# Performance work log

Hardware: AMD Instinct MI355X
Metric: run time of the kernel (lower is better)

## Reference

```python
import jax, jax.numpy as jnp
import numpy as np

B, M, NT, V, D, H, E, S = 4, 12, 12, 10000, 64, 3, 512, 32


def setup_inputs() -> dict:
    key = jax.random.key(0)
    ks = jax.random.split(key, 16)
    def rn(k, shape, scale=0.05):
        return jax.random.normal(k, shape, dtype=jnp.float32) * scale
    return {
        "tendency": jax.random.normal(ks[0], (B, M, V), dtype=jnp.float32),
        "periodicity": jax.random.normal(ks[1], (B, NT, V), dtype=jnp.float32),
        "edges": jax.random.randint(ks[2], (H, E, S), 0, V),
        "w1": rn(ks[3], (1, D)), "b1": rn(ks[4], (D,)),
        "w2": rn(ks[5], (D, D)), "b2": rn(ks[6], (D,)),
        "attn_w": rn(ks[7], (D, D)), "attn_a": rn(ks[8], (2 * D, 1)),
        "w_ih": rn(ks[9], (4 * D, D)), "w_hh": rn(ks[10], (4 * D, D)),
        "b_ih": rn(ks[11], (4 * D,)), "b_hh": rn(ks[12], (4 * D,)),
        "w_out": rn(ks[13], (2 * D, 1)), "b_out": rn(ks[14], (1,)),
    }


def _hypersage(X, edges, w, b):
    # X: (N, V, F); edges: (E, S) node indices. All edges have size S <= Q,
    # so torch's random subsampling is the identity.
    n, v, f = X.shape
    e, s = edges.shape
    gathered = X[:, edges, :]                      # (N, E, S, F)
    agg = gathered.mean(axis=2)                    # (N, E, F)
    flat = edges.reshape(-1)                       # (E*S,)
    contrib = jnp.broadcast_to(agg[:, :, None, :], (n, e, s, f)).reshape(n, e * s, f)
    X_out = jnp.zeros((n, v, f), X.dtype).at[:, flat, :].add(contrib)
    deg = jnp.zeros((v,), X.dtype).at[flat].add(1.0)
    deg = jnp.maximum(deg, 1.0)
    X_out = X_out / deg[None, :, None]
    return X_out @ w + b                           # Linear fc


def _attention(Xs, attn_w, attn_a):
    # Xs: (H, N, V, D)
    ref = Xs.mean(axis=0)                          # (N, V, D)
    wx = Xs @ attn_w                               # (H, N, V, D)
    wr = ref @ attn_w                              # (N, V, D)
    z = jnp.concatenate([wx, jnp.broadcast_to(wr[None], wx.shape)], axis=-1) @ attn_a
    z = jax.nn.leaky_relu(z, negative_slope=0.2)   # (H, N, V, 1)
    alpha = jax.nn.softmax(z, axis=0)
    return (alpha * Xs).sum(axis=0)                # (N, V, D)


def _lstm_final(x, w_ih, w_hh, b_ih, b_hh):
    # x: (BV, T, D) -> final hidden state (BV, D). PyTorch gate order i,f,g,o.
    bv, t, d = x.shape
    xg = x @ w_ih.T + (b_ih + b_hh)                # precompute input gates (BV, T, 4D)
    def step(carry, xg_t):
        h, c = carry
        g = xg_t + h @ w_hh.T
        i, f, gg, o = jnp.split(g, 4, axis=-1)
        c = jax.nn.sigmoid(f) * c + jax.nn.sigmoid(i) * jnp.tanh(gg)
        h = jax.nn.sigmoid(o) * jnp.tanh(c)
        return (h, c), None
    h0 = jnp.zeros((bv, d), x.dtype)
    (h, _), _ = jax.lax.scan(step, (h0, h0), jnp.swapaxes(xg, 0, 1))
    return h


def _branch(seq, edges, w1, b1, w2, b2, attn_w, attn_a, w_ih, w_hh, b_ih, b_hh):
    b, t, v = seq.shape
    X = seq.reshape(b * t, v, 1)                   # fold time into batch (same DAMHG per step)
    def per_hg(e):
        return _hypersage(_hypersage(X, e, w1, b1), e, w2, b2)
    xs = jax.vmap(per_hg)(edges)                   # (H, B*T, V, D)
    fused = _attention(xs, attn_w, attn_a)         # (B*T, V, D)
    d = fused.shape[-1]
    seq_v = fused.reshape(b, t, v, d).transpose(0, 2, 1, 3).reshape(b * v, t, d)
    h = _lstm_final(seq_v, w_ih, w_hh, b_ih, b_hh)
    return h.reshape(b, v, d)


def reference(tendency, periodicity, edges, w1, b1, w2, b2, attn_w, attn_a, w_ih, w_hh, b_ih, b_hh, w_out, b_out):
    h_t = _branch(tendency, edges, w1, b1, w2, b2, attn_w, attn_a, w_ih, w_hh, b_ih, b_hh)
    h_p = _branch(periodicity, edges, w1, b1, w2, b2, attn_w, attn_a, w_ih, w_hh, b_ih, b_hh)
    fusion = jnp.concatenate([h_t, h_p], axis=-1)  # (B, V, 2D)
    out = fusion @ w_out + b_out                   # (B, V, 1)
    return out[..., 0]
```

## Files before the change

### kernel.cpp

```cpp
#include <hip/hip_runtime.h>

#define NV 10000
#define NB 4
#define NTT 12
#define NSEQ 48
#define NH 3
#define NE 512
#define NS 32
#define ND 64

#define S_U   0
#define S_C1  64
#define S_V1  128
#define S_V2  192
#define S_SC  256
#define S_GU  272
#define S_GC  528
#define S_G0  784
#define F_INV 1040
#define F_M   (F_INV + NH*NV)
#define F_PQ  (F_M + NH*NV)
#define F_HT  (F_PQ + 4*NV*NSEQ)
#define I_CNT (F_HT + 2*NB*NV)
#define I_CUR (I_CNT + NH*NV)
#define I_OFF (I_CUR + NH*NV)
#define I_SLOT (I_OFF + NH*NV)
#define F_DYN (I_SLOT + NH*NE*NS)
#define XT_SZ  (NV*NSEQ)
#define AGG_SZ (NH*NE*NSEQ)
#define YZ_SZ  (NH*NV*NSEQ)

typedef __attribute__((ext_vector_type(8))) _Float16 f16x8;
typedef __attribute__((ext_vector_type(4))) float f32x4;

__device__ __forceinline__ float sigf(float x) {
  return __builtin_amdgcn_rcpf(1.0f + __expf(-x));
}
__device__ __forceinline__ unsigned short f2h(float x) {
  union { _Float16 h; unsigned short u; } c;
  c.h = (_Float16)x;
  return c.u;
}
__device__ __forceinline__ f16x8 ldsH(const unsigned short* p) {
  union { uint4 u; f16x8 v; } x;
  x.u = *(const uint4*)p;
  return x.v;
}

__global__ void k_prep(const float* __restrict__ w1, const float* __restrict__ b1,
                       const float* __restrict__ w2, const float* __restrict__ b2,
                       const float* __restrict__ attn_w, const float* __restrict__ attn_a,
                       const float* __restrict__ w_ih, const float* __restrict__ b_ih,
                       const float* __restrict__ b_hh, float* __restrict__ ws) {
  __shared__ float u_s[64], c1_s[64];
  const int tid = threadIdx.x;
  if (tid < 64) {
    float v1 = 0.f, v2 = 0.f, u = 0.f, c1 = 0.f;
    for (int d = 0; d < 64; ++d) {
      const float aw = attn_w[tid * 64 + d];
      v1 += aw * attn_a[d];
      v2 += aw * attn_a[64 + d];
      const float w2v = w2[d * 64 + tid];
      u  += w1[d] * w2v;
      c1 += b1[d] * w2v;
    }
    ws[S_U + tid] = u;  ws[S_C1 + tid] = c1;
    ws[S_V1 + tid] = v1; ws[S_V2 + tid] = v2;
    u_s[tid] = u; c1_s[tid] = c1;
  }
  __syncthreads();
  if (tid == 0) {
    float al = 0.f, be = 0.f, ga = 0.f, de = 0.f, ep = 0.f;
    for (int d = 0; d < 64; ++d) {
      const float v1 = ws[S_V1 + d], v2 = ws[S_V2 + d];
      al += u_s[d] * v1;  be += c1_s[d] * v1;
      ga += u_s[d] * v2;  de += c1_s[d] * v2;
      ep += b2[d] * (v1 + v2);
    }
    ws[S_SC + 0] = al; ws[S_SC + 1] = be; ws[S_SC + 2] = ga;
    ws[S_SC + 3] = de; ws[S_SC + 4] = ep;
  }
  {
    const int j = tid;
    float gu = 0.f, gc = 0.f, g0 = 0.f;
    for (int d = 0; d < 64; ++d) {
      const float w = w_ih[j * 64 + d];
      gu += w * u_s[d]; gc += w * c1_s[d]; g0 += w * b2[d];
    }
    ws[S_GU + j] = gu; ws[S_GC + j] = gc;
    ws[S_G0 + j] = g0 + b_ih[j] + b_hh[j];
  }
}

__global__ void k_zero(int* __restrict__ p, int n) {
  const int g = blockIdx.x * 256 + threadIdx.x;
  if (g < n) p[g] = 0;
}

__global__ void k_count(const int* __restrict__ edges, int* __restrict__ counts) {
  const int g = blockIdx.x * 256 + threadIdx.x;
  if (g >= NH * NE * NS) return;
  const int h = g >> 14;
  atomicAdd(&counts[h * NV + edges[g]], 1);
}

__global__ void k_scan(const int* __restrict__ counts, int* __restrict__ offs,
                       float* __restrict__ invdeg, float* __restrict__ mvec) {
  const int h = blockIdx.x;
  const int tid = threadIdx.x;
  const int base = h * NV;
  const int CH = 10;
  int local[10];
  int run = 0;
  for (int i = 0; i < CH; ++i) {
    const int v = tid * CH + i;
    const int c = (v < NV) ? counts[base + v] : 0;
    local[i] = run; run += c;
  }
  __shared__ int sd[1024];
  sd[tid] = run;
  __syncthreads();
  int acc = run;
  for (int off = 1; off < 1024; off <<= 1) {
    const int t = (tid >= off) ? sd[tid - off] : 0;
    __syncthreads();
    acc += t; sd[tid] = acc;
    __syncthreads();
  }
  const int excl = acc - run;
  for (int i = 0; i < CH; ++i) {
    const int v = tid * CH + i;
    if (v < NV) {
      offs[base + v] = excl + local[i];
      const int c = counts[base + v];
      invdeg[base + v] = 1.0f / (float)((c > 0) ? c : 1);
      mvec[base + v] = (c > 0) ? 1.0f : 0.0f;
    }
  }
}

__global__ void k_fill(const int* __restrict__ edges, const int* __restrict__ offs,
                       int* __restrict__ cursor, int* __restrict__ slot_edge) {
  const int g = blockIdx.x * 256 + threadIdx.x;
  if (g >= NH * NE * NS) return;
  const int h = g >> 14;
  const int e = (g >> 5) & (NE - 1);
  const int v = edges[g];
  const int pos = atomicAdd(&cursor[h * NV + v], 1);
  slot_edge[h * NE * NS + offs[h * NV + v] + pos] = e;
}

__global__ void k_trans2(const float* __restrict__ s0, const float* __restrict__ s1,
                         float* __restrict__ xT, int xtS) {
  __shared__ float tile[128][49];
  const float* seq = blockIdx.y ? s1 : s0;
  float* o = xT + (size_t)blockIdx.y * xtS;
  const int v0 = blockIdx.x * 128;
  const int tid = threadIdx.x;
  for (int i = tid; i < 128 * NSEQ; i += 256) {
    const int n = i / 128, vl = i % 128;
    const int v = v0 + vl;
    tile[vl][n] = (v < NV) ? seq[n * NV + v] : 0.0f;
  }
  __syncthreads();
  for (int i = tid; i < 128 * NSEQ; i += 256) {
    const int vl = i / NSEQ, n = i % NSEQ;
    const int v = v0 + vl;
    if (v < NV) o[v * NSEQ + n] = tile[vl][n];
  }
}

__global__ void k_eagg1(const int* __restrict__ edges, const float* __restrict__ xT,
                        int xtS, float* __restrict__ agg, int aggS) {
  const int g = blockIdx.x * 256 + threadIdx.x;
  if (g >= NH * NE * 12) return;
  const float* x = xT + (size_t)blockIdx.y * xtS;
  float* a = agg + (size_t)blockIdx.y * aggS;
  const int n0 = (g % 12) * 4;
  const int e = (g / 12) % NE;
  const int h = g / (12 * NE);
  const int* ep = edges + (h * NE + e) * NS;
  float4 acc = make_float4(0.f, 0.f, 0.f, 0.f);
  for (int s = 0; s < NS; ++s) {
    const float4 t = *(const float4*)&x[ep[s] * NSEQ + n0];
    acc.x += t.x; acc.y += t.y; acc.z += t.z; acc.w += t.w;
  }
  acc.x *= (1.0f / NS); acc.y *= (1.0f / NS); acc.z *= (1.0f / NS); acc.w *= (1.0f / NS);
  *(float4*)&a[(h * NE + e) * NSEQ + n0] = acc;
}

__global__ void k_eagg2(const int* __restrict__ edges, const float* __restrict__ ysum,
                        int yS, const float* __restrict__ invdeg,
                        float* __restrict__ agg, int aggS) {
  const int g = blockIdx.x * 256 + threadIdx.x;
  if (g >= NH * NE * 12) return;
  const float* y = ysum + (size_t)blockIdx.y * yS;
  float* a = agg + (size_t)blockIdx.y * aggS;
  const int n0 = (g % 12) * 4;
  const int e = (g / 12) % NE;
  const int h = g / (12 * NE);
  const int* ep = edges + (h * NE + e) * NS;
  float4 acc = make_float4(0.f, 0.f, 0.f, 0.f);
  for (int s = 0; s < NS; ++s) {
    const int v = ep[s];
    const float iv = invdeg[h * NV + v];
    const float4 t = *(const float4*)&y[(h * NV + v) * NSEQ + n0];
    acc.x += t.x * iv; acc.y += t.y * iv; acc.z += t.z * iv; acc.w += t.w * iv;
  }
  acc.x *= (1.0f / NS); acc.y *= (1.0f / NS); acc.z *= (1.0f / NS); acc.w *= (1.0f / NS);
  *(float4*)&a[(h * NE + e) * NSEQ + n0] = acc;
}

__global__ void k_vg(const int* __restrict__ counts, const int* __restrict__ offs,
                     const int* __restrict__ slot_edge, const float* __restrict__ agg,
                     int aggS, float* __restrict__ outv, int outS) {
  const int g = blockIdx.x * 256 + threadIdx.x;
  if (g >= NH * NV * 12) return;
  const float* a = agg + (size_t)blockIdx.y * aggS;
  float* o = outv + (size_t)blockIdx.y * outS;
  const int n0 = (g % 12) * 4;
  const int v = (g / 12) % NV;
  const int h = g / (12 * NV);
  const int beg = offs[h * NV + v];
  const int cnt = counts[h * NV + v];
  const int* se = slot_edge + h * NE * NS;
  float4 acc = make_float4(0.f, 0.f, 0.f, 0.f);
  for (int i = 0; i < cnt; ++i) {
    const int e = se[beg + i];
    const float4 t = *(const float4*)&a[(h * NE + e) * NSEQ + n0];
    acc.x += t.x; acc.y += t.y; acc.z += t.z; acc.w += t.w;
  }
  *(float4*)&o[(h * NV + v) * NSEQ + n0] = acc;
}

__global__ void k_attn(const float* __restrict__ zsum, int zS,
                       const float* __restrict__ invdeg, const float* __restrict__ mvec,
                       const float* __restrict__ ws, float* __restrict__ pq, int br0) {
  const int g = blockIdx.x * 256 + threadIdx.x;
  if (g >= NV * 12) return;
  const int bi = blockIdx.y;
  const float* z = zsum + (size_t)bi * zS;
  float* pbuf = pq + (size_t)(bi + br0) * 2 * NV * NSEQ;
  float* qbuf = pbuf + NV * NSEQ;
  const int n0 = (g % 12) * 4;
  const int v = g / 12;
  const float al = ws[S_SC + 0], be = ws[S_SC + 1], ga = ws[S_SC + 2],
              de = ws[S_SC + 3], ep = ws[S_SC + 4];
  union { float4 v4; float f[4]; } zh[3], pv, qv;
  float mh[3];
  #pragma unroll
  for (int h = 0; h < NH; ++h) {
    const float iv = invdeg[h * NV + v];
    float4 t = *(const float4*)&z[(h * NV + v) * NSEQ + n0];
    t.x *= iv; t.y *= iv; t.z *= iv; t.w *= iv;
    zh[h].v4 = t;
    mh[h] = mvec[h * NV + v];
  }
  const float mb = (mh[0] + mh[1] + mh[2]) * (1.f / 3.f);
  #pragma unroll
  for (int j = 0; j < 4; ++j) {
    const float z0 = zh[0].f[j], z1 = zh[1].f[j], z2 = zh[2].f[j];
    const float zb = (z0 + z1 + z2) * (1.f / 3.f);
    float sc[3];
    const float zt[3] = {z0, z1, z2};
    #pragma unroll
    for (int h = 0; h < NH; ++h) {
      const float s = al * zt[h] + be * mh[h] + ga * zb + de * mb + ep;
      sc[h] = (s > 0.f) ? s : 0.2f * s;
    }
    const float mx = fmaxf(sc[0], fmaxf(sc[1], sc[2]));
    const float e0 = __expf(sc[0] - mx), e1 = __expf(sc[1] - mx), e2 = __expf(sc[2] - mx);
    const float inv = 1.0f / (e0 + e1 + e2);
    pv.f[j] = (e0 * z0 + e1 * z1 + e2 * z2) * inv;
    qv.f[j] = (e0 * mh[0] + e1 * mh[1] + e2 * mh[2]) * inv;
  }
  *(float4*)&pbuf[v * NSEQ + n0] = pv.v4;
  *(float4*)&qbuf[v * NSEQ + n0] = qv.v4;
}

#define RS2 72
__launch_bounds__(256, 4)
__global__ void k_lstm2(const float* __restrict__ w_hh, const float* __restrict__ ws,
                        const float* __restrict__ pbase, const float* __restrict__ w_out,
                        float* __restrict__ part) {
  __shared__ __align__(16) unsigned short smem[2 * 64 * RS2];
  __shared__ float ps_sh[NTT][64], qs_sh[NTT][64];
  const int tid = threadIdx.x;
  const int w = tid >> 6, lane = tid & 63, q = lane >> 4, l15 = lane & 15;
  const int b = blockIdx.y, br = blockIdx.z;
  const int v0 = blockIdx.x * 64;
  const int d = w * 16 + l15;

  union HU { uint4 u; f16x8 v; };

  const float* pp = pbase + (size_t)br * 2 * NV * NSEQ;
  const float* qq = pp + NV * NSEQ;
  for (int i = tid; i < 384; i += 256) {
    const int arr = (i >= 192) ? 1 : 0;
    const int ii = i - arr * 192;
    const int s = ii / 3, f4 = ii % 3;
    const int v = v0 + s;
    const float* src = arr ? qq : pp;
    float4 val = make_float4(0.f, 0.f, 0.f, 0.f);
    if (v < NV) val = *(const float4*)&src[v * NSEQ + b * NTT + f4 * 4];
    float (*dst)[64] = arr ? qs_sh : ps_sh;
    dst[f4 * 4 + 0][s] = val.x; dst[f4 * 4 + 1][s] = val.y;
    dst[f4 * 4 + 2][s] = val.z; dst[f4 * 4 + 3][s] = val.w;
  }

  f16x8 Bf[4][2];
  #pragma unroll
  for (int g = 0; g < 4; ++g)
    #pragma unroll
    for (int kh = 0; kh < 2; ++kh) {
      const float* wp = w_hh + (g * 64 + d) * 64 + kh * 32 + q * 8;
      const float4 lo = *(const float4*)wp;
      const float4 hi = *(const float4*)(wp + 4);
      HU f;
      f.u.x = (unsigned int)f2h(lo.x) | ((unsigned int)f2h(lo.y) << 16);
      f.u.y = (unsigned int)f2h(lo.z) | ((unsigned int)f2h(lo.w) << 16);
      f.u.z = (unsigned int)f2h(hi.x) | ((unsigned int)f2h(hi.y) << 16);
      f.u.w = (unsigned int)f2h(hi.z) | ((unsigned int)f2h(hi.w) << 16);
      Bf[g][kh] = f.v;
    }

  HU bex[4];
  #pragma unroll
  for (int g = 0; g < 4; ++g) {
    const float gu = ws[S_GU + g * 64 + d];
    const float gc = ws[S_GC + g * 64 + d];
    const float g0 = ws[S_G0 + g * 64 + d];
    bex[g].u.x = (q == 0) ? ((unsigned int)f2h(gu) | ((unsigned int)f2h(gc) << 16)) : 0u;
    bex[g].u.y = (q == 0) ? (unsigned int)f2h(g0) : 0u;
    bex[g].u.z = 0u; bex[g].u.w = 0u;
  }
  const float WO = w_out[br * 64 + d];
  __syncthreads();

  f32x4 cst[4];
  float pr[4][4];
  #pragma unroll
  for (int mi = 0; mi < 4; ++mi) cst[mi] = (f32x4){0.f, 0.f, 0.f, 0.f};
  const f32x4 z4 = (f32x4){0.f, 0.f, 0.f, 0.f};

  #pragma unroll 1
  for (int t = 0; t < NTT; ++t) {
    const unsigned short* hr = smem + ((t + 1) & 1) * (64 * RS2);
    unsigned short* hw = smem + (t & 1) * (64 * RS2);
    const bool last = (t == NTT - 1);
    #pragma unroll
    for (int mi = 0; mi < 4; ++mi) {
      HU ae;
      const float pv = ps_sh[t][mi * 16 + l15];
      const float qv = qs_sh[t][mi * 16 + l15];
      ae.u.x = (q == 0) ? ((unsigned int)f2h(pv) | ((unsigned int)f2h(qv) << 16)) : 0u;
      ae.u.y = (q == 0) ? 0x3C00u : 0u;
      ae.u.z = 0u; ae.u.w = 0u;
      f32x4 aI = __builtin_amdgcn_mfma_f32_16x16x32_f16(ae.v, bex[0].v, z4, 0, 0, 0);
      f32x4 aF = __builtin_amdgcn_mfma_f32_16x16x32_f16(ae.v, bex[1].v, z4, 0, 0, 0);
      f32x4 aG = __builtin_amdgcn_mfma_f32_16x16x32_f16(ae.v, bex[2].v, z4, 0, 0, 0);
      f32x4 aO = __builtin_amdgcn_mfma_f32_16x16x32_f16(ae.v, bex[3].v, z4, 0, 0, 0);
      if (t > 0) {
        #pragma unroll
        for (int kh = 0; kh < 2; ++kh) {
          const f16x8 Ah = ldsH(&hr[(mi * 16 + l15) * RS2 + kh * 32 + q * 8]);
          aI = __builtin_amdgcn_mfma_f32_16x16x32_f16(Ah, Bf[0][kh], aI, 0, 0, 0);
          aF = __builtin_amdgcn_mfma_f32_16x16x32_f16(Ah, Bf[1][kh], aF, 0, 0, 0);
          aG = __builtin_amdgcn_mfma_f32_16x16x32_f16(Ah, Bf[2][kh], aG, 0, 0, 0);
          aO = __builtin_amdgcn_mfma_f32_16x16x32_f16(Ah, Bf[3][kh], aO, 0, 0, 0);
        }
      }
      #pragma unroll
      for (int r = 0; r < 4; ++r) {
        const float ea = __expf(-aI[r]);
        const float eb = __expf(-2.0f * aG[r]);
        const float igg = (1.0f - eb) *
            __builtin_amdgcn_rcpf((1.0f + ea) * (1.0f + eb));
        const float fg = sigf(aF[r]);
        const float cn = fmaf(fg, cst[mi][r], igg);
        cst[mi][r] = cn;
        const float ec = __expf(-aO[r]);
        const float ed = __expf(-2.0f * cn);
        const float h = (1.0f - ed) *
            __builtin_amdgcn_rcpf((1.0f + ec) * (1.0f + ed));
        if (!last) {
          hw[(mi * 16 + q * 4 + r) * RS2 + d] = f2h(h);
        } else {
          pr[mi][r] = h * WO;
        }
      }
    }
    __syncthreads();
  }
  float* fbuf = (float*)smem;
  #pragma unroll
  for (int mi = 0; mi < 4; ++mi)
    #pragma unroll
    for (int r = 0; r < 4; ++r) {
      float v = pr[mi][r];
      v += __shfl_xor(v, 1);
      v += __shfl_xor(v, 2);
      v += __shfl_xor(v, 4);
      v += __shfl_xor(v, 8);
      if (l15 == 0) fbuf[w * 64 + mi * 16 + q * 4 + r] = v;
    }
  __syncthreads();
  if (tid < 64) {
    const int v = v0 + tid;
    if (v < NV)
      part[(br * NB + b) * NV + v] =
          fbuf[tid] + fbuf[64 + tid] + fbuf[128 + tid] + fbuf[192 + tid];
  }
}

__global__ void k_comb(const float* __restrict__ part, const float* __restrict__ b_out,
                       float* __restrict__ out) {
  const int g = blockIdx.x * 256 + threadIdx.x;
  if (g >= NB * NV / 4) return;
  const float4 a = ((const float4*)part)[g];
  const float4 c = ((const float4*)part)[NB * NV / 4 + g];
  const float bo = b_out[0];
  float4 o;
  o.x = a.x + c.x + bo; o.y = a.y + c.y + bo;
  o.z = a.z + c.z + bo; o.w = a.w + c.w + bo;
  ((float4*)out)[g] = o;
}

extern "C" void kernel_launch(void* const* d_in, const int* in_sizes, int n_in,
                              void* d_out, int out_size, void* d_ws, size_t ws_size,
                              hipStream_t stream) {
  const float* tend   = (const float*)d_in[0];
  const float* peri   = (const float*)d_in[1];
  const int*   edges  = (const int*)d_in[2];
  const float* w1     = (const float*)d_in[3];
  const float* b1     = (const float*)d_in[4];
  const float* w2     = (const float*)d_in[5];
  const float* b2     = (const float*)d_in[6];
  const float* attn_w = (const float*)d_in[7];
  const float* attn_a = (const float*)d_in[8];
  const float* w_ih   = (const float*)d_in[9];
  const float* w_hh   = (const float*)d_in[10];
  const float* b_ih   = (const float*)d_in[11];
  const float* b_hh   = (const float*)d_in[12];
  const float* w_out  = (const float*)d_in[13];
  const float* b_out  = (const float*)d_in[14];
  float* out = (float*)d_out;
  float* ws  = (float*)d_ws;
  int*   iws = (int*)d_ws;
  int* cnt = iws + I_CNT;
  int* cur = iws + I_CUR;
  int* off = iws + I_OFF;
  int* sed = iws + I_SLOT;

  const size_t need2 = ((size_t)F_DYN + 2 * (XT_SZ + AGG_SZ + YZ_SZ)) * 4;
  const bool batched = ws_size >= need2;
  const int nb = batched ? 2 : 1;
  float* XT  = ws + F_DYN;
  float* AGG = XT + (size_t)nb * XT_SZ;
  float* YZ  = AGG + (size_t)nb * AGG_SZ;

  k_prep<<<1, 256, 0, stream>>>(w1, b1, w2, b2, attn_w, attn_a, w_ih, b_ih, b_hh, ws);
  k_zero<<<(2 * NH * NV + 255) / 256, 256, 0, stream>>>(cnt, 2 * NH * NV);
  k_count<<<(NH * NE * NS) / 256, 256, 0, stream>>>(edges, cnt);
  k_scan<<<NH, 1024, 0, stream>>>(cnt, off, ws + F_INV, ws + F_M);
  k_fill<<<(NH * NE * NS) / 256, 256, 0, stream>>>(edges, off, cur, sed);

  const int g_eagg = (NH * NE * 12 + 255) / 256;
  const int g_vg   = (NH * NV * 12 + 255) / 256;
  const int g_attn = (NV * 12 + 255) / 256;
  if (batched) {
    k_trans2<<<dim3((NV + 127) / 128, 2), 256, 0, stream>>>(tend, peri, XT, XT_SZ);
    k_eagg1<<<dim3(g_eagg, 2), 256, 0, stream>>>(edges, XT, XT_SZ, AGG, AGG_SZ);
    k_vg<<<dim3(g_vg, 2), 256, 0, stream>>>(cnt, off, sed, AGG, AGG_SZ, YZ, YZ_SZ);
    k_eagg2<<<dim3(g_eagg, 2), 256, 0, stream>>>(edges, YZ, YZ_SZ, ws + F_INV, AGG, AGG_SZ);
    k_vg<<<dim3(g_vg, 2), 256, 0, stream>>>(cnt, off, sed, AGG, AGG_SZ, YZ, YZ_SZ);
    k_attn<<<dim3(g_attn, 2), 256, 0, stream>>>(YZ, YZ_SZ, ws + F_INV, ws + F_M, ws, ws + F_PQ, 0);
  } else {
    for (int br = 0; br < 2; ++br) {
      const float* seq = br ? peri : tend;
      k_trans2<<<dim3((NV + 127) / 128, 1), 256, 0, stream>>>(seq, seq, XT, 0);
      k_eagg1<<<dim3(g_eagg, 1), 256, 0, stream>>>(edges, XT, 0, AGG, 0);
      k_vg<<<dim3(g_vg, 1), 256, 0, stream>>>(cnt, off, sed, AGG, 0, YZ, 0);
      k_eagg2<<<dim3(g_eagg, 1), 256, 0, stream>>>(edges, YZ, 0, ws + F_INV, AGG, 0);
      k_vg<<<dim3(g_vg, 1), 256, 0, stream>>>(cnt, off, sed, AGG, 0, YZ, 0);
      k_attn<<<dim3(g_attn, 1), 256, 0, stream>>>(YZ, 0, ws + F_INV, ws + F_M, ws, ws + F_PQ, br);
    }
  }
  dim3 lgrid((NV + 63) / 64, NB, 2);
  k_lstm2<<<lgrid, 256, 0, stream>>>(w_hh, ws, ws + F_PQ, w_out, ws + F_HT);
  k_comb<<<(NB * NV / 4 + 255) / 256, 256, 0, stream>>>(ws + F_HT, b_out, out);
}
```

Before: 256.9 us.

## Fuse vertex gather into attention, pack p/q as fp16, batch two sequences per LSTM block

The second vertex-gather kernel is folded into the attention kernel, so the per-hyperedge sums are aggregated and scored in one pass. This drops the YZ intermediate write and read along with one launch. The attention output (p,q) is now stored as packed fp16 pairs, which halves that buffer's traffic and lets the LSTM load MFMA operands directly without converting. Each LSTM block now handles two batch elements with interleaved recurrences, giving more independent MFMA work per synchronisation. This costs more LDS and registers, hence the lower launch bound. The cell update also merges the sigmoid reciprocals into a single rcp.

```diff
diff --git a/kernel.cpp b/kernel.cpp
--- a/kernel.cpp
+++ b/kernel.cpp
@@ -33,9 +33,6 @@
 typedef __attribute__((ext_vector_type(8))) _Float16 f16x8;
 typedef __attribute__((ext_vector_type(4))) float f32x4;
 
-__device__ __forceinline__ float sigf(float x) {
-  return __builtin_amdgcn_rcpf(1.0f + __expf(-x));
-}
 __device__ __forceinline__ unsigned short f2h(float x) {
   union { _Float16 h; unsigned short u; } c;
   c.h = (_Float16)x;
@@ -233,30 +230,40 @@
   *(float4*)&o[(h * NV + v) * NSEQ + n0] = acc;
 }
 
-__global__ void k_attn(const float* __restrict__ zsum, int zS,
-                       const float* __restrict__ invdeg, const float* __restrict__ mvec,
-                       const float* __restrict__ ws, float* __restrict__ pq, int br0) {
+__global__ void k_vgattn(const int* __restrict__ counts, const int* __restrict__ offs,
+                         const int* __restrict__ slot_edge, const float* __restrict__ agg,
+                         int aggS, const float* __restrict__ invdeg,
+                         const float* __restrict__ mvec, const float* __restrict__ ws,
+                         unsigned int* __restrict__ pq, int br0) {
   const int g = blockIdx.x * 256 + threadIdx.x;
   if (g >= NV * 12) return;
   const int bi = blockIdx.y;
-  const float* z = zsum + (size_t)bi * zS;
-  float* pbuf = pq + (size_t)(bi + br0) * 2 * NV * NSEQ;
-  float* qbuf = pbuf + NV * NSEQ;
+  const float* a = agg + (size_t)bi * aggS;
+  unsigned int* pbuf = pq + (size_t)(bi + br0) * NV * NSEQ;
   const int n0 = (g % 12) * 4;
   const int v = g / 12;
   const float al = ws[S_SC + 0], be = ws[S_SC + 1], ga = ws[S_SC + 2],
               de = ws[S_SC + 3], ep = ws[S_SC + 4];
-  union { float4 v4; float f[4]; } zh[3], pv, qv;
+  union { float4 v4; float f[4]; } zh[3];
   float mh[3];
   #pragma unroll
   for (int h = 0; h < NH; ++h) {
+    const int beg = offs[h * NV + v];
+    const int cnt = counts[h * NV + v];
+    const int* se = slot_edge + h * NE * NS;
+    float4 acc = make_float4(0.f, 0.f, 0.f, 0.f);
+    for (int i = 0; i < cnt; ++i) {
+      const int e = se[beg + i];
+      const float4 t = *(const float4*)&a[(h * NE + e) * NSEQ + n0];
+      acc.x += t.x; acc.y += t.y; acc.z += t.z; acc.w += t.w;
+    }
     const float iv = invdeg[h * NV + v];
-    float4 t = *(const float4*)&z[(h * NV + v) * NSEQ + n0];
-    t.x *= iv; t.y *= iv; t.z *= iv; t.w *= iv;
-    zh[h].v4 = t;
+    zh[h].v4 = make_float4(acc.x * iv, acc.y * iv, acc.z * iv, acc.w * iv);
     mh[h] = mvec[h * NV + v];
   }
   const float mb = (mh[0] + mh[1] + mh[2]) * (1.f / 3.f);
+  uint4 o4;
+  unsigned int* op = (unsigned int*)&o4;
   #pragma unroll
   for (int j = 0; j < 4; ++j) {
     const float z0 = zh[0].f[j], z1 = zh[1].f[j], z2 = zh[2].f[j];
@@ -271,41 +278,37 @@
     const float mx = fmaxf(sc[0], fmaxf(sc[1], sc[2]));
     const float e0 = __expf(sc[0] - mx), e1 = __expf(sc[1] - mx), e2 = __expf(sc[2] - mx);
     const float inv = 1.0f / (e0 + e1 + e2);
-    pv.f[j] = (e0 * z0 + e1 * z1 + e2 * z2) * inv;
-    qv.f[j] = (e0 * mh[0] + e1 * mh[1] + e2 * mh[2]) * inv;
-  }
-  *(float4*)&pbuf[v * NSEQ + n0] = pv.v4;
-  *(float4*)&qbuf[v * NSEQ + n0] = qv.v4;
+    const float pv = (e0 * z0 + e1 * z1 + e2 * z2) * inv;
+    const float qv = (e0 * mh[0] + e1 * mh[1] + e2 * mh[2]) * inv;
+    op[j] = (unsigned int)f2h(pv) | ((unsigned int)f2h(qv) << 16);
+  }
+  *(uint4*)&pbuf[v * NSEQ + n0] = o4;
 }
 
 #define RS2 72
-__launch_bounds__(256, 4)
+__launch_bounds__(256, 3)
 __global__ void k_lstm2(const float* __restrict__ w_hh, const float* __restrict__ ws,
-                        const float* __restrict__ pbase, const float* __restrict__ w_out,
-                        float* __restrict__ part) {
-  __shared__ __align__(16) unsigned short smem[2 * 64 * RS2];
-  __shared__ float ps_sh[NTT][64], qs_sh[NTT][64];
+                        const unsigned int* __restrict__ pqbase,
+                        const float* __restrict__ w_out, float* __restrict__ part) {
+  __shared__ __align__(16) unsigned short smem[4 * 64 * RS2];
+  __shared__ unsigned int pq_sh[2][NTT][64];
   const int tid = threadIdx.x;
   const int w = tid >> 6, lane = tid & 63, q = lane >> 4, l15 = lane & 15;
-  const int b = blockIdx.y, br = blockIdx.z;
+  const int b0 = blockIdx.y * 2, br = blockIdx.z;
   const int v0 = blockIdx.x * 64;
   const int d = w * 16 + l15;
 
   union HU { uint4 u; f16x8 v; };
 
-  const float* pp = pbase + (size_t)br * 2 * NV * NSEQ;
-  const float* qq = pp + NV * NSEQ;
+  const unsigned int* pqb = pqbase + (size_t)br * NV * NSEQ;
   for (int i = tid; i < 384; i += 256) {
-    const int arr = (i >= 192) ? 1 : 0;
-    const int ii = i - arr * 192;
+    const int u = i / 192, ii = i % 192;
     const int s = ii / 3, f4 = ii % 3;
     const int v = v0 + s;
-    const float* src = arr ? qq : pp;
-    float4 val = make_float4(0.f, 0.f, 0.f, 0.f);
-    if (v < NV) val = *(const float4*)&src[v * NSEQ + b * NTT + f4 * 4];
-    float (*dst)[64] = arr ? qs_sh : ps_sh;
-    dst[f4 * 4 + 0][s] = val.x; dst[f4 * 4 + 1][s] = val.y;
-    dst[f4 * 4 + 2][s] = val.z; dst[f4 * 4 + 3][s] = val.w;
+    uint4 val = make_uint4(0u, 0u, 0u, 0u);
+    if (v < NV) val = *(const uint4*)&pqb[v * NSEQ + (b0 + u) * NTT + f4 * 4];
+    pq_sh[u][f4 * 4 + 0][s] = val.x; pq_sh[u][f4 * 4 + 1][s] = val.y;
+    pq_sh[u][f4 * 4 + 2][s] = val.z; pq_sh[u][f4 * 4 + 3][s] = val.w;
   }
 
   f16x8 Bf[4][2];
@@ -337,79 +340,88 @@
   const float WO = w_out[br * 64 + d];
   __syncthreads();
 
-  f32x4 cst[4];
-  float pr[4][4];
+  f32x4 cst[2][4];
+  float pr[2][4][4];
   #pragma unroll
-  for (int mi = 0; mi < 4; ++mi) cst[mi] = (f32x4){0.f, 0.f, 0.f, 0.f};
+  for (int u = 0; u < 2; ++u)
+    #pragma unroll
+    for (int mi = 0; mi < 4; ++mi) cst[u][mi] = (f32x4){0.f, 0.f, 0.f, 0.f};
   const f32x4 z4 = (f32x4){0.f, 0.f, 0.f, 0.f};
 
   #pragma unroll 1
   for (int t = 0; t < NTT; ++t) {
-    const unsigned short* hr = smem + ((t + 1) & 1) * (64 * RS2);
-    unsigned short* hw = smem + (t & 1) * (64 * RS2);
     const bool last = (t == NTT - 1);
     #pragma unroll
-    for (int mi = 0; mi < 4; ++mi) {
-      HU ae;
-      const float pv = ps_sh[t][mi * 16 + l15];
-      const float qv = qs_sh[t][mi * 16 + l15];
-      ae.u.x = (q == 0) ? ((unsigned int)f2h(pv) | ((unsigned int)f2h(qv) << 16)) : 0u;
-      ae.u.y = (q == 0) ? 0x3C00u : 0u;
-      ae.u.z = 0u; ae.u.w = 0u;
-      f32x4 aI = __builtin_amdgcn_mfma_f32_16x16x32_f16(ae.v, bex[0].v, z4, 0, 0, 0);
-      f32x4 aF = __builtin_amdgcn_mfma_f32_16x16x32_f16(ae.v, bex[1].v, z4, 0, 0, 0);
-      f32x4 aG = __builtin_amdgcn_mfma_f32_16x16x32_f16(ae.v, bex[2].v, z4, 0, 0, 0);
-      f32x4 aO = __builtin_amdgcn_mfma_f32_16x16x32_f16(ae.v, bex[3].v, z4, 0, 0, 0);
-      if (t > 0) {
+    for (int u = 0; u < 2; ++u) {
+      const unsigned short* hr = smem + (u * 2 + ((t + 1) & 1)) * (64 * RS2);
+      unsigned short* hw = smem + (u * 2 + (t & 1)) * (64 * RS2);
+      #pragma unroll
+      for (int mi = 0; mi < 4; ++mi) {
+        HU ae;
+        ae.u.x = (q == 0) ? pq_sh[u][t][mi * 16 + l15] : 0u;
+        ae.u.y = (q == 0) ? 0x3C00u : 0u;
+        ae.u.z = 0u; ae.u.w = 0u;
+        f32x4 aI = __builtin_amdgcn_mfma_f32_16x16x32_f16(ae.v, bex[0].v, z4, 0, 0, 0);
+        f32x4 aF = __builtin_amdgcn_mfma_f32_16x16x32_f16(ae.v, bex[1].v, z4, 0, 0, 0);
+        f32x4 aG = __builtin_amdgcn_mfma_f32_16x16x32_f16(ae.v, bex[2].v, z4, 0, 0, 0);
+        f32x4 aO = __builtin_amdgcn_mfma_f32_16x16x32_f16(ae.v, bex[3].v, z4, 0, 0, 0);
+        if (t > 0) {
+          #pragma unroll
+          for (int kh = 0; kh < 2; ++kh) {
+            const f16x8 Ah = ldsH(&hr[(mi * 16 + l15) * RS2 + kh * 32 + q * 8]);
+            aI = __builtin_amdgcn_mfma_f32_16x16x32_f16(Ah, Bf[0][kh], aI, 0, 0, 0);
+            aF = __builtin_amdgcn_mfma_f32_16x16x32_f16(Ah, Bf[1][kh], aF, 0, 0, 0);
+            aG = __builtin_amdgcn_mfma_f32_16x16x32_f16(Ah, Bf[2][kh], aG, 0, 0, 0);
+            aO = __builtin_amdgcn_mfma_f32_16x16x32_f16(Ah, Bf[3][kh], aO, 0, 0, 0);
+          }
+        }
         #pragma unroll
-        for (int kh = 0; kh < 2; ++kh) {
-          const f16x8 Ah = ldsH(&hr[(mi * 16 + l15) * RS2 + kh * 32 + q * 8]);
-          aI = __builtin_amdgcn_mfma_f32_16x16x32_f16(Ah, Bf[0][kh], aI, 0, 0, 0);
-          aF = __builtin_amdgcn_mfma_f32_16x16x32_f16(Ah, Bf[1][kh], aF, 0, 0, 0);
-          aG = __builtin_amdgcn_mfma_f32_16x16x32_f16(Ah, Bf[2][kh], aG, 0, 0, 0);
-          aO = __builtin_amdgcn_mfma_f32_16x16x32_f16(Ah, Bf[3][kh], aO, 0, 0, 0);
+        for (int r = 0; r < 4; ++r) {
+          const float c  = cst[u][mi][r];
+          const float ea = __expf(-aI[r]);
+          const float eb = __expf(-2.0f * aG[r]);
+          const float ef = __expf(-aF[r]);
+          const float A  = 1.0f + ea, Bb = 1.0f + eb, Fd = 1.0f + ef;
+          const float P  = A * Bb;
+          const float numer = fmaf(c, P, (1.0f - eb) * Fd);
+          const float cn = numer * __builtin_amdgcn_rcpf(Fd * P);
+          cst[u][mi][r] = cn;
+          const float ec = __expf(-aO[r]);
+          const float ed = __expf(-2.0f * cn);
+          const float h = (1.0f - ed) *
+              __builtin_amdgcn_rcpf((1.0f + ec) * (1.0f + ed));
+          if (!last) {
+            hw[(mi * 16 + q * 4 + r) * RS2 + d] = f2h(h);
+          } else {
+            pr[u][mi][r] = h * WO;
+          }
         }
       }
+    }
+    __syncthreads();
+  }
+  float* fbuf = (float*)smem;
+  #pragma unroll
+  for (int u = 0; u < 2; ++u)
+    #pragma unroll
+    for (int mi = 0; mi < 4; ++mi)
       #pragma unroll
       for (int r = 0; r < 4; ++r) {
-        const float ea = __expf(-aI[r]);
-        const float eb = __expf(-2.0f * aG[r]);
-        const float igg = (1.0f - eb) *
-            __builtin_amdgcn_rcpf((1.0f + ea) * (1.0f + eb));
-        const float fg = sigf(aF[r]);
-        const float cn = fmaf(fg, cst[mi][r], igg);
-        cst[mi][r] = cn;
-        const float ec = __expf(-aO[r]);
-        const float ed = __expf(-2.0f * cn);
-        const float h = (1.0f - ed) *
-            __builtin_amdgcn_rcpf((1.0f + ec) * (1.0f + ed));
-        if (!last) {
-          hw[(mi * 16 + q * 4 + r) * RS2 + d] = f2h(h);
-        } else {
-          pr[mi][r] = h * WO;
-        }
+        float v = pr[u][mi][r];
+        v += __shfl_xor(v, 1);
+        v += __shfl_xor(v, 2);
+        v += __shfl_xor(v, 4);
+        v += __shfl_xor(v, 8);
+        if (l15 == 0) fbuf[u * 256 + w * 64 + mi * 16 + q * 4 + r] = v;
       }
-    }
-    __syncthreads();
-  }
-  float* fbuf = (float*)smem;
-  #pragma unroll
-  for (int mi = 0; mi < 4; ++mi)
-    #pragma unroll
-    for (int r = 0; r < 4; ++r) {
-      float v = pr[mi][r];
-      v += __shfl_xor(v, 1);
-      v += __shfl_xor(v, 2);
-      v += __shfl_xor(v, 4);
-      v += __shfl_xor(v, 8);
-      if (l15 == 0) fbuf[w * 64 + mi * 16 + q * 4 + r] = v;
-    }
   __syncthreads();
-  if (tid < 64) {
-    const int v = v0 + tid;
-    if (v < NV)
-      part[(br * NB + b) * NV + v] =
-          fbuf[tid] + fbuf[64 + tid] + fbuf[128 + tid] + fbuf[192 + tid];
+  if (tid < 128) {
+    const int u = tid >> 6, s = tid & 63;
+    const int v = v0 + s;
+    if (v < NV) {
+      const float* fb = fbuf + u * 256;
+      part[(br * NB + (b0 + u)) * NV + v] = fb[s] + fb[64 + s] + fb[128 + s] + fb[192 + s];
+    }
   }
 }
 
@@ -451,6 +463,7 @@
   int* cur = iws + I_CUR;
   int* off = iws + I_OFF;
   int* sed = iws + I_SLOT;
+  unsigned int* pqw = (unsigned int*)(ws + F_PQ);
 
   const size_t need2 = ((size_t)F_DYN + 2 * (XT_SZ + AGG_SZ + YZ_SZ)) * 4;
   const bool batched = ws_size >= need2;
@@ -473,8 +486,8 @@
     k_eagg1<<<dim3(g_eagg, 2), 256, 0, stream>>>(edges, XT, XT_SZ, AGG, AGG_SZ);
     k_vg<<<dim3(g_vg, 2), 256, 0, stream>>>(cnt, off, sed, AGG, AGG_SZ, YZ, YZ_SZ);
     k_eagg2<<<dim3(g_eagg, 2), 256, 0, stream>>>(edges, YZ, YZ_SZ, ws + F_INV, AGG, AGG_SZ);
-    k_vg<<<dim3(g_vg, 2), 256, 0, stream>>>(cnt, off, sed, AGG, AGG_SZ, YZ, YZ_SZ);
-    k_attn<<<dim3(g_attn, 2), 256, 0, stream>>>(YZ, YZ_SZ, ws + F_INV, ws + F_M, ws, ws + F_PQ, 0);
+    k_vgattn<<<dim3(g_attn, 2), 256, 0, stream>>>(cnt, off, sed, AGG, AGG_SZ,
+                                                  ws + F_INV, ws + F_M, ws, pqw, 0);
   } else {
     for (int br = 0; br < 2; ++br) {
       const float* seq = br ? peri : tend;
@@ -482,11 +495,11 @@
       k_eagg1<<<dim3(g_eagg, 1), 256, 0, stream>>>(edges, XT, 0, AGG, 0);
       k_vg<<<dim3(g_vg, 1), 256, 0, stream>>>(cnt, off, sed, AGG, 0, YZ, 0);
       k_eagg2<<<dim3(g_eagg, 1), 256, 0, stream>>>(edges, YZ, 0, ws + F_INV, AGG, 0);
-      k_vg<<<dim3(g_vg, 1), 256, 0, stream>>>(cnt, off, sed, AGG, 0, YZ, 0);
-      k_attn<<<dim3(g_attn, 1), 256, 0, stream>>>(YZ, 0, ws + F_INV, ws + F_M, ws, ws + F_PQ, br);
-    }
-  }
-  dim3 lgrid((NV + 63) / 64, NB, 2);
-  k_lstm2<<<lgrid, 256, 0, stream>>>(w_hh, ws, ws + F_PQ, w_out, ws + F_HT);
+      k_vgattn<<<dim3(g_attn, 1), 256, 0, stream>>>(cnt, off, sed, AGG, 0,
+                                                    ws + F_INV, ws + F_M, ws, pqw, br);
+    }
+  }
+  dim3 lgrid((NV + 63) / 64, NB / 2, 2);
+  k_lstm2<<<lgrid, 256, 0, stream>>>(w_hh, ws, pqw, w_out, ws + F_HT);
   k_comb<<<(NB * NV / 4 + 255) / 256, 256, 0, stream>>>(ws + F_HT, b_out, out);
 }
```

After: 265.5 us. 1.03x slower.
